# Performance work log

Hardware: AMD Instinct MI355X
Metric: run time of the kernel (lower is better)

The kernel has to match this reference:

```python
import jax, jax.numpy as jnp
import numpy as np

N = 10000
E = 640000
C = 128   # in_channels
H = 512   # hidden_dim
O = 128   # out_channels


def setup_inputs() -> dict:
    key = jax.random.key(0)
    k1, k2, k3, k4, k5, k6, k7 = jax.random.split(key, 7)
    x = jax.random.normal(k1, (N, C), dtype=jnp.float32)
    edge_index = jax.random.randint(k2, (2, E), 0, N, dtype=jnp.int64)
    # MLP params (Linear(2C, H) -> ReLU -> Linear(H, O)), torch default init scale
    w1 = jax.random.uniform(k3, (2 * C, H), jnp.float32, -1, 1) / np.sqrt(2 * C)
    b1 = jax.random.uniform(k4, (H,), jnp.float32, -1, 1) / np.sqrt(2 * C)
    w2 = jax.random.uniform(k5, (H, O), jnp.float32, -1, 1) / np.sqrt(H)
    b2 = jax.random.uniform(k6, (O,), jnp.float32, -1, 1) / np.sqrt(H)
    return {"x": x, "edge_index": edge_index, "w1": w1, "b1": b1, "w2": w2, "b2": b2}


def reference(x, edge_index, w1, b1, w2, b2):
    row, col = edge_index[0], edge_index[1]
    # scatter_mean: mean of source features x[col] into destination row
    summed = jax.ops.segment_sum(x[col], row, num_segments=N)          # [N, C]
    count = jax.ops.segment_sum(jnp.ones((E,), x.dtype), row, num_segments=N)
    neighbor_mean = summed / jnp.maximum(count, 1.0)[:, None]          # [N, C]
    h = jnp.concatenate([x, neighbor_mean], axis=1)                    # [N, 2C]
    h = jax.nn.relu(h @ w1 + b1)                                       # [N, H]
    return h @ w2 + b2                                                 # [N, O]
```

## Files before the change

kernel.cpp:

```cpp
#include <hip/hip_runtime.h>

#define C_IN 128
#define H_DIM 512
#define O_DIM 128
#define CAP   128
#define PAD   16
#define BM    32

typedef __attribute__((ext_vector_type(8))) short short8;
typedef __attribute__((ext_vector_type(4))) float f32x4;

__device__ inline unsigned short f2bf(float f) {
    unsigned int u = __float_as_uint(f);
    unsigned int r = (u + 0x7FFF + ((u >> 16) & 1)) >> 16;
    return (unsigned short)r;
}
__device__ inline float bf2f(unsigned short s) {
    return __uint_as_float(((unsigned int)s) << 16);
}

__device__ inline void tr_tile(const float* __restrict__ src, unsigned short* __restrict__ dst,
                               int R, int Ccols, int bx, int by) {
    __shared__ float tile[32][33];
    const int c0 = bx * 32, r0 = by * 32;
    const int tx = threadIdx.x & 31, ty = threadIdx.x >> 5;
#pragma unroll
    for (int i = 0; i < 32; i += 8)
        tile[ty + i][tx] = src[(long)(r0 + ty + i) * Ccols + c0 + tx];
    __syncthreads();
#pragma unroll
    for (int i = 0; i < 32; i += 8)
        dst[(long)(c0 + ty + i) * R + r0 + tx] = f2bf(tile[tx][ty + i]);
}

__global__ __launch_bounds__(256)
void prep_kernel(const float* __restrict__ w1, unsigned short* __restrict__ w1t,
                 const float* __restrict__ w2, unsigned short* __restrict__ w2t,
                 const float* __restrict__ x, unsigned short* __restrict__ h0,
                 int* __restrict__ cnt_p, int N) {
    if (blockIdx.z == 0) {
        if (blockIdx.y < (2 * C_IN) / 32) tr_tile(w1, w1t, 2 * C_IN, H_DIM, blockIdx.x, blockIdx.y);
    } else if (blockIdx.z == 1) {
        if (blockIdx.x < O_DIM / 32) tr_tile(w2, w2t, H_DIM, O_DIM, blockIdx.x, blockIdx.y);
    } else {
        const int bid = blockIdx.y * 16 + blockIdx.x;
        const int gtid = bid * 256 + threadIdx.x;
        const int nf4 = N * C_IN / 4;
        for (int i = gtid; i < nf4; i += 65536) {
            int n = i >> 5, c4 = i & 31;
            float4 v = ((const float4*)x)[i];
            ushort4 s;
            s.x = f2bf(v.x); s.y = f2bf(v.y); s.z = f2bf(v.z); s.w = f2bf(v.w);
            *(ushort4*)(h0 + (long)n * (2 * C_IN) + c4 * 4) = s;
        }
        const int n4 = N * PAD / 4;
        for (int i = gtid; i < n4; i += 65536)
            ((int4*)cnt_p)[i] = make_int4(0, 0, 0, 0);
    }
}

__global__ void fill_kernel(const int* __restrict__ ei, int* __restrict__ cnt_p,
                            unsigned short* __restrict__ bucket, int E) {
    int e = (blockIdx.x * blockDim.x + threadIdx.x) * 4;
    if (((E & 3) == 0) && e < E) {
        int4 r = *(const int4*)(ei + e);
        int4 c = *(const int4*)(ei + E + e);
        int s0 = atomicAdd(&cnt_p[r.x * PAD], 1);
        int s1 = atomicAdd(&cnt_p[r.y * PAD], 1);
        int s2 = atomicAdd(&cnt_p[r.z * PAD], 1);
        int s3 = atomicAdd(&cnt_p[r.w * PAD], 1);
        if (s0 < CAP) bucket[(long)r.x * CAP + s0] = (unsigned short)c.x;
        if (s1 < CAP) bucket[(long)r.y * CAP + s1] = (unsigned short)c.y;
        if (s2 < CAP) bucket[(long)r.z * CAP + s2] = (unsigned short)c.z;
        if (s3 < CAP) bucket[(long)r.w * CAP + s3] = (unsigned short)c.w;
    } else {
        for (int k = e; k < E && k < e + 4; k++) {
            int row = ei[k];
            int col = ei[E + k];
            int slot = atomicAdd(&cnt_p[row * PAD], 1);
            if (slot < CAP) bucket[(long)row * CAP + slot] = (unsigned short)col;
        }
    }
}

__global__ __launch_bounds__(256)
void gather_kernel(const unsigned short* __restrict__ bucket,
                   const int* __restrict__ cnt_p, unsigned short* __restrict__ h0,
                   int N) {
    const int lane = threadIdx.x & 63;
    const int n = blockIdx.x * 4 + (threadIdx.x >> 6);
    if (n >= N) return;
    const int g = lane >> 4;
    const int l16 = lane & 15;
    const int degt = cnt_p[n * PAD];
    const int deg = min(degt, CAP);

    const unsigned int bb = ((const unsigned int*)bucket)[(long)n * (CAP / 2) + lane];

    float acc[8] = {};
    int e = 0;
    for (; e + 16 <= deg; e += 16) {
        int k0 = e + g, k1 = e + 4 + g, k2 = e + 8 + g, k3 = e + 12 + g;
        int c0 = (__shfl(bb, k0 >> 1) >> ((k0 & 1) << 4)) & 0xffff;
        int c1 = (__shfl(bb, k1 >> 1) >> ((k1 & 1) << 4)) & 0xffff;
        int c2 = (__shfl(bb, k2 >> 1) >> ((k2 & 1) << 4)) & 0xffff;
        int c3 = (__shfl(bb, k3 >> 1) >> ((k3 & 1) << 4)) & 0xffff;
        short8 u0 = *(const short8*)(h0 + (long)c0 * (2 * C_IN) + l16 * 8);
        short8 u1 = *(const short8*)(h0 + (long)c1 * (2 * C_IN) + l16 * 8);
        short8 u2 = *(const short8*)(h0 + (long)c2 * (2 * C_IN) + l16 * 8);
        short8 u3 = *(const short8*)(h0 + (long)c3 * (2 * C_IN) + l16 * 8);
#pragma unroll
        for (int j = 0; j < 8; j++)
            acc[j] += (bf2f((unsigned short)u0[j]) + bf2f((unsigned short)u1[j]))
                    + (bf2f((unsigned short)u2[j]) + bf2f((unsigned short)u3[j]));
    }
    if (e + 8 <= deg) {
        int k0 = e + g, k1 = e + 4 + g;
        int c0 = (__shfl(bb, k0 >> 1) >> ((k0 & 1) << 4)) & 0xffff;
        int c1 = (__shfl(bb, k1 >> 1) >> ((k1 & 1) << 4)) & 0xffff;
        short8 u0 = *(const short8*)(h0 + (long)c0 * (2 * C_IN) + l16 * 8);
        short8 u1 = *(const short8*)(h0 + (long)c1 * (2 * C_IN) + l16 * 8);
#pragma unroll
        for (int j = 0; j < 8; j++)
            acc[j] += bf2f((unsigned short)u0[j]) + bf2f((unsigned short)u1[j]);
        e += 8;
    }
    if (e + 4 <= deg) {
        int k = e + g;
        int c = (__shfl(bb, k >> 1) >> ((k & 1) << 4)) & 0xffff;
        short8 u = *(const short8*)(h0 + (long)c * (2 * C_IN) + l16 * 8);
#pragma unroll
        for (int j = 0; j < 8; j++) acc[j] += bf2f((unsigned short)u[j]);
        e += 4;
    }
    {
        int rem = deg - e;
        int k = e + g;
        unsigned int bv = __shfl(bb, k >> 1);
        if (g < rem) {
            int c = (bv >> ((k & 1) << 4)) & 0xffff;
            short8 u = *(const short8*)(h0 + (long)c * (2 * C_IN) + l16 * 8);
#pragma unroll
            for (int j = 0; j < 8; j++) acc[j] += bf2f((unsigned short)u[j]);
        }
    }
#pragma unroll
    for (int j = 0; j < 8; j++) {
        acc[j] += __shfl_xor(acc[j], 16, 64);
        acc[j] += __shfl_xor(acc[j], 32, 64);
    }
    if (lane < 16) {
        float inv = 1.0f / fmaxf((float)degt, 1.0f);
        short8 mv;
#pragma unroll
        for (int j = 0; j < 8; j++) mv[j] = (short)f2bf(acc[j] * inv);
        *(short8*)(h0 + (long)n * (2 * C_IN) + C_IN + l16 * 8) = mv;
    }
}

__global__ __launch_bounds__(256, 3)
void fused_mlp(const unsigned short* __restrict__ h0,
               const unsigned short* __restrict__ w1t,
               const float* __restrict__ bias1,
               const unsigned short* __restrict__ w2t,
               const float* __restrict__ bias2,
               float* __restrict__ out, int M) {
    __shared__ __align__(16) unsigned short h1s[BM][520];

    const int t = threadIdx.x;
    const int m0 = blockIdx.x * BM;
    const int lane = t & 63;
    const int w = t >> 6;
    const int l16 = lane & 15;
    const int q = lane >> 4;
    const int q8 = q * 8;

    short8 a_reg[2][8];
#pragma unroll
    for (int mf = 0; mf < 2; mf++) {
        int gm = m0 + mf * 16 + l16;
        if (gm < M) {
            const unsigned short* ap = h0 + (long)gm * (2 * C_IN) + q8;
#pragma unroll
            for (int s = 0; s < 8; s++) a_reg[mf][s] = *(const short8*)(ap + s * 32);
        } else {
#pragma unroll
            for (int s = 0; s < 8; s++) a_reg[mf][s] = short8{};
        }
    }

#pragma unroll
    for (int nc = 0; nc < 4; nc++) {
        const int colbase = w * 128 + nc * 32;
        f32x4 acc[2][2] = {};
#pragma unroll
        for (int s = 0; s < 8; s++) {
            short8 b0 = *(const short8*)(w1t + (long)(colbase + l16) * 256 + s * 32 + q8);
            short8 b1 = *(const short8*)(w1t + (long)(colbase + 16 + l16) * 256 + s * 32 + q8);
            acc[0][0] = __builtin_amdgcn_mfma_f32_16x16x32_bf16(a_reg[0][s], b0, acc[0][0], 0, 0, 0);
            acc[0][1] = __builtin_amdgcn_mfma_f32_16x16x32_bf16(a_reg[0][s], b1, acc[0][1], 0, 0, 0);
            acc[1][0] = __builtin_amdgcn_mfma_f32_16x16x32_bf16(a_reg[1][s], b0, acc[1][0], 0, 0, 0);
            acc[1][1] = __builtin_amdgcn_mfma_f32_16x16x32_bf16(a_reg[1][s], b1, acc[1][1], 0, 0, 0);
        }
        float bb0 = bias1[colbase + l16];
        float bb1 = bias1[colbase + 16 + l16];
#pragma unroll
        for (int mf = 0; mf < 2; mf++) {
#pragma unroll
            for (int r = 0; r < 4; r++) {
                int m = mf * 16 + q * 4 + r;
                h1s[m][colbase + l16]      = f2bf(fmaxf(acc[mf][0][r] + bb0, 0.f));
                h1s[m][colbase + 16 + l16] = f2bf(fmaxf(acc[mf][1][r] + bb1, 0.f));
            }
        }
    }
    __syncthreads();

    f32x4 acc2[2][2] = {};
    const int wn = w * 32;
#pragma unroll
    for (int ks = 0; ks < 16; ks++) {
        short8 a0 = *(const short8*)&h1s[l16][ks * 32 + q8];
        short8 a1 = *(const short8*)&h1s[16 + l16][ks * 32 + q8];
        short8 b0 = *(const short8*)(w2t + (long)(wn + l16) * H_DIM + ks * 32 + q8);
        short8 b1 = *(const short8*)(w2t + (long)(wn + 16 + l16) * H_DIM + ks * 32 + q8);
        acc2[0][0] = __builtin_amdgcn_mfma_f32_16x16x32_bf16(a0, b0, acc2[0][0], 0, 0, 0);
        acc2[0][1] = __builtin_amdgcn_mfma_f32_16x16x32_bf16(a0, b1, acc2[0][1], 0, 0, 0);
        acc2[1][0] = __builtin_amdgcn_mfma_f32_16x16x32_bf16(a1, b0, acc2[1][0], 0, 0, 0);
        acc2[1][1] = __builtin_amdgcn_mfma_f32_16x16x32_bf16(a1, b1, acc2[1][1], 0, 0, 0);
    }
#pragma unroll
    for (int mf = 0; mf < 2; mf++) {
#pragma unroll
        for (int nf = 0; nf < 2; nf++) {
            int gn = wn + nf * 16 + l16;
            float bb = bias2[gn];
#pragma unroll
            for (int r = 0; r < 4; r++) {
                int gm = m0 + mf * 16 + q * 4 + r;
                if (gm < M) out[(long)gm * O_DIM + gn] = acc2[mf][nf][r] + bb;
            }
        }
    }
}

extern "C" void kernel_launch(void* const* d_in, const int* in_sizes, int n_in,
                              void* d_out, int out_size, void* d_ws, size_t ws_size,
                              hipStream_t stream) {
    const float* x  = (const float*)d_in[0];
    const int*   ei = (const int*)d_in[1];
    const float* w1 = (const float*)d_in[2];
    const float* b1 = (const float*)d_in[3];
    const float* w2 = (const float*)d_in[4];
    const float* b2 = (const float*)d_in[5];
    float* out = (float*)d_out;

    const int N = in_sizes[0] / C_IN;
    const int E = in_sizes[1] / 2;

    unsigned short* h0b = (unsigned short*)d_ws;
    unsigned short* w1t = h0b + (size_t)N * (2 * C_IN);
    unsigned short* w2t = w1t + (size_t)H_DIM * (2 * C_IN);
    int* cnt_p = (int*)(w2t + (size_t)O_DIM * H_DIM);
    unsigned short* bucket = (unsigned short*)(cnt_p + (size_t)N * PAD);

    prep_kernel<<<dim3(16, 16, 3), 256, 0, stream>>>(w1, w1t, w2, w2t, x, h0b, cnt_p, N);
    fill_kernel<<<(E / 4 + 255) / 256, 256, 0, stream>>>(ei, cnt_p, bucket, E);
    gather_kernel<<<(N + 3) / 4, 256, 0, stream>>>(bucket, cnt_p, h0b, N);
    fused_mlp<<<(N + BM - 1) / BM, 256, 0, stream>>>(h0b, w1t, b1, w2t, b2, out, N);
}
```

Baseline: 140.9 us.

## Fuse all stages into one persistent kernel with software grid barriers

The four launches (prep, fill, gather, MLP) become a single persistent kernel of 768 blocks. The stages are separated by atomic-counter grid barriers, and the counter zeroing moves to a hipMemsetAsync. This removes the launch gaps and tail idle between kernels. In exchange it depends on all 768 blocks being resident at once (3 per CU on 256 CUs). The barrier also has a guard timeout that could silently break ordering, and every stage now runs on a fixed grid size.

```diff
diff --git a/kernel.cpp b/kernel.cpp
--- a/kernel.cpp
+++ b/kernel.cpp
@@ -6,6 +6,7 @@
 #define CAP   128
 #define PAD   16
 #define BM    32
+#define NBLK  768
 
 typedef __attribute__((ext_vector_type(8))) short short8;
 typedef __attribute__((ext_vector_type(4))) float f32x4;
@@ -19,9 +20,24 @@
     return __uint_as_float(((unsigned int)s) << 16);
 }
 
-__device__ inline void tr_tile(const float* __restrict__ src, unsigned short* __restrict__ dst,
+__device__ inline void gbar(int* bar, int nblk) {
+    __syncthreads();
+    __builtin_amdgcn_fence(__ATOMIC_RELEASE, "agent");
+    if (threadIdx.x == 0) {
+        __hip_atomic_fetch_add(bar, 1, __ATOMIC_RELAXED, __HIP_MEMORY_SCOPE_AGENT);
+        int guard = 0;
+        while (__hip_atomic_load(bar, __ATOMIC_RELAXED, __HIP_MEMORY_SCOPE_AGENT) < nblk) {
+            __builtin_amdgcn_s_sleep(8);
+            if (++guard > (1 << 22)) break;
+        }
+    }
+    __syncthreads();
+    __builtin_amdgcn_fence(__ATOMIC_ACQUIRE, "agent");
+}
+
+__device__ inline void tr_tile(float (*tile)[33], const float* __restrict__ src,
+                               unsigned short* __restrict__ dst,
                                int R, int Ccols, int bx, int by) {
-    __shared__ float tile[32][33];
     const int c0 = bx * 32, r0 = by * 32;
     const int tx = threadIdx.x & 31, ty = threadIdx.x >> 5;
 #pragma unroll
@@ -31,216 +47,220 @@
 #pragma unroll
     for (int i = 0; i < 32; i += 8)
         dst[(long)(c0 + ty + i) * R + r0 + tx] = f2bf(tile[tx][ty + i]);
-}
-
-__global__ __launch_bounds__(256)
-void prep_kernel(const float* __restrict__ w1, unsigned short* __restrict__ w1t,
-                 const float* __restrict__ w2, unsigned short* __restrict__ w2t,
-                 const float* __restrict__ x, unsigned short* __restrict__ h0,
-                 int* __restrict__ cnt_p, int N) {
-    if (blockIdx.z == 0) {
-        if (blockIdx.y < (2 * C_IN) / 32) tr_tile(w1, w1t, 2 * C_IN, H_DIM, blockIdx.x, blockIdx.y);
-    } else if (blockIdx.z == 1) {
-        if (blockIdx.x < O_DIM / 32) tr_tile(w2, w2t, H_DIM, O_DIM, blockIdx.x, blockIdx.y);
-    } else {
-        const int bid = blockIdx.y * 16 + blockIdx.x;
-        const int gtid = bid * 256 + threadIdx.x;
-        const int nf4 = N * C_IN / 4;
-        for (int i = gtid; i < nf4; i += 65536) {
-            int n = i >> 5, c4 = i & 31;
-            float4 v = ((const float4*)x)[i];
-            ushort4 s;
-            s.x = f2bf(v.x); s.y = f2bf(v.y); s.z = f2bf(v.z); s.w = f2bf(v.w);
-            *(ushort4*)(h0 + (long)n * (2 * C_IN) + c4 * 4) = s;
-        }
-        const int n4 = N * PAD / 4;
-        for (int i = gtid; i < n4; i += 65536)
-            ((int4*)cnt_p)[i] = make_int4(0, 0, 0, 0);
-    }
-}
-
-__global__ void fill_kernel(const int* __restrict__ ei, int* __restrict__ cnt_p,
-                            unsigned short* __restrict__ bucket, int E) {
-    int e = (blockIdx.x * blockDim.x + threadIdx.x) * 4;
-    if (((E & 3) == 0) && e < E) {
-        int4 r = *(const int4*)(ei + e);
-        int4 c = *(const int4*)(ei + E + e);
-        int s0 = atomicAdd(&cnt_p[r.x * PAD], 1);
-        int s1 = atomicAdd(&cnt_p[r.y * PAD], 1);
-        int s2 = atomicAdd(&cnt_p[r.z * PAD], 1);
-        int s3 = atomicAdd(&cnt_p[r.w * PAD], 1);
-        if (s0 < CAP) bucket[(long)r.x * CAP + s0] = (unsigned short)c.x;
-        if (s1 < CAP) bucket[(long)r.y * CAP + s1] = (unsigned short)c.y;
-        if (s2 < CAP) bucket[(long)r.z * CAP + s2] = (unsigned short)c.z;
-        if (s3 < CAP) bucket[(long)r.w * CAP + s3] = (unsigned short)c.w;
-    } else {
-        for (int k = e; k < E && k < e + 4; k++) {
-            int row = ei[k];
-            int col = ei[E + k];
-            int slot = atomicAdd(&cnt_p[row * PAD], 1);
-            if (slot < CAP) bucket[(long)row * CAP + slot] = (unsigned short)col;
-        }
-    }
-}
-
-__global__ __launch_bounds__(256)
-void gather_kernel(const unsigned short* __restrict__ bucket,
-                   const int* __restrict__ cnt_p, unsigned short* __restrict__ h0,
-                   int N) {
-    const int lane = threadIdx.x & 63;
-    const int n = blockIdx.x * 4 + (threadIdx.x >> 6);
-    if (n >= N) return;
-    const int g = lane >> 4;
-    const int l16 = lane & 15;
-    const int degt = cnt_p[n * PAD];
-    const int deg = min(degt, CAP);
-
-    const unsigned int bb = ((const unsigned int*)bucket)[(long)n * (CAP / 2) + lane];
-
-    float acc[8] = {};
-    int e = 0;
-    for (; e + 16 <= deg; e += 16) {
-        int k0 = e + g, k1 = e + 4 + g, k2 = e + 8 + g, k3 = e + 12 + g;
-        int c0 = (__shfl(bb, k0 >> 1) >> ((k0 & 1) << 4)) & 0xffff;
-        int c1 = (__shfl(bb, k1 >> 1) >> ((k1 & 1) << 4)) & 0xffff;
-        int c2 = (__shfl(bb, k2 >> 1) >> ((k2 & 1) << 4)) & 0xffff;
-        int c3 = (__shfl(bb, k3 >> 1) >> ((k3 & 1) << 4)) & 0xffff;
-        short8 u0 = *(const short8*)(h0 + (long)c0 * (2 * C_IN) + l16 * 8);
-        short8 u1 = *(const short8*)(h0 + (long)c1 * (2 * C_IN) + l16 * 8);
-        short8 u2 = *(const short8*)(h0 + (long)c2 * (2 * C_IN) + l16 * 8);
-        short8 u3 = *(const short8*)(h0 + (long)c3 * (2 * C_IN) + l16 * 8);
-#pragma unroll
-        for (int j = 0; j < 8; j++)
-            acc[j] += (bf2f((unsigned short)u0[j]) + bf2f((unsigned short)u1[j]))
-                    + (bf2f((unsigned short)u2[j]) + bf2f((unsigned short)u3[j]));
-    }
-    if (e + 8 <= deg) {
-        int k0 = e + g, k1 = e + 4 + g;
-        int c0 = (__shfl(bb, k0 >> 1) >> ((k0 & 1) << 4)) & 0xffff;
-        int c1 = (__shfl(bb, k1 >> 1) >> ((k1 & 1) << 4)) & 0xffff;
-        short8 u0 = *(const short8*)(h0 + (long)c0 * (2 * C_IN) + l16 * 8);
-        short8 u1 = *(const short8*)(h0 + (long)c1 * (2 * C_IN) + l16 * 8);
-#pragma unroll
-        for (int j = 0; j < 8; j++)
-            acc[j] += bf2f((unsigned short)u0[j]) + bf2f((unsigned short)u1[j]);
-        e += 8;
-    }
-    if (e + 4 <= deg) {
-        int k = e + g;
-        int c = (__shfl(bb, k >> 1) >> ((k & 1) << 4)) & 0xffff;
-        short8 u = *(const short8*)(h0 + (long)c * (2 * C_IN) + l16 * 8);
-#pragma unroll
-        for (int j = 0; j < 8; j++) acc[j] += bf2f((unsigned short)u[j]);
-        e += 4;
-    }
-    {
-        int rem = deg - e;
-        int k = e + g;
-        unsigned int bv = __shfl(bb, k >> 1);
-        if (g < rem) {
-            int c = (bv >> ((k & 1) << 4)) & 0xffff;
-            short8 u = *(const short8*)(h0 + (long)c * (2 * C_IN) + l16 * 8);
-#pragma unroll
-            for (int j = 0; j < 8; j++) acc[j] += bf2f((unsigned short)u[j]);
-        }
-    }
-#pragma unroll
-    for (int j = 0; j < 8; j++) {
-        acc[j] += __shfl_xor(acc[j], 16, 64);
-        acc[j] += __shfl_xor(acc[j], 32, 64);
-    }
-    if (lane < 16) {
-        float inv = 1.0f / fmaxf((float)degt, 1.0f);
-        short8 mv;
-#pragma unroll
-        for (int j = 0; j < 8; j++) mv[j] = (short)f2bf(acc[j] * inv);
-        *(short8*)(h0 + (long)n * (2 * C_IN) + C_IN + l16 * 8) = mv;
-    }
+    __syncthreads();
 }
 
 __global__ __launch_bounds__(256, 3)
-void fused_mlp(const unsigned short* __restrict__ h0,
-               const unsigned short* __restrict__ w1t,
-               const float* __restrict__ bias1,
-               const unsigned short* __restrict__ w2t,
-               const float* __restrict__ bias2,
-               float* __restrict__ out, int M) {
+void fused_all(const float* __restrict__ x, const int* __restrict__ ei,
+               const float* __restrict__ w1, const float* __restrict__ bias1,
+               const float* __restrict__ w2, const float* __restrict__ bias2,
+               unsigned short* __restrict__ h0, unsigned short* __restrict__ w1t,
+               unsigned short* __restrict__ w2t, int* __restrict__ cnt_p,
+               unsigned short* __restrict__ bucket, int* __restrict__ bar,
+               float* __restrict__ out, int N, int E) {
+    __shared__ float tile[32][33];
     __shared__ __align__(16) unsigned short h1s[BM][520];
 
+    const int bid = blockIdx.x;
+    const int nblk = gridDim.x;
     const int t = threadIdx.x;
-    const int m0 = blockIdx.x * BM;
     const int lane = t & 63;
-    const int w = t >> 6;
+    const int wv = t >> 6;
     const int l16 = lane & 15;
     const int q = lane >> 4;
     const int q8 = q * 8;
 
-    short8 a_reg[2][8];
-#pragma unroll
-    for (int mf = 0; mf < 2; mf++) {
-        int gm = m0 + mf * 16 + l16;
-        if (gm < M) {
-            const unsigned short* ap = h0 + (long)gm * (2 * C_IN) + q8;
-#pragma unroll
-            for (int s = 0; s < 8; s++) a_reg[mf][s] = *(const short8*)(ap + s * 32);
+    for (int job = bid; job < 192; job += nblk) {
+        if (job < 128) {
+            tr_tile(tile, w1, w1t, 2 * C_IN, H_DIM, job & 15, job >> 4);
         } else {
-#pragma unroll
-            for (int s = 0; s < 8; s++) a_reg[mf][s] = short8{};
-        }
-    }
-
-#pragma unroll
-    for (int nc = 0; nc < 4; nc++) {
-        const int colbase = w * 128 + nc * 32;
-        f32x4 acc[2][2] = {};
-#pragma unroll
-        for (int s = 0; s < 8; s++) {
-            short8 b0 = *(const short8*)(w1t + (long)(colbase + l16) * 256 + s * 32 + q8);
-            short8 b1 = *(const short8*)(w1t + (long)(colbase + 16 + l16) * 256 + s * 32 + q8);
-            acc[0][0] = __builtin_amdgcn_mfma_f32_16x16x32_bf16(a_reg[0][s], b0, acc[0][0], 0, 0, 0);
-            acc[0][1] = __builtin_amdgcn_mfma_f32_16x16x32_bf16(a_reg[0][s], b1, acc[0][1], 0, 0, 0);
-            acc[1][0] = __builtin_amdgcn_mfma_f32_16x16x32_bf16(a_reg[1][s], b0, acc[1][0], 0, 0, 0);
-            acc[1][1] = __builtin_amdgcn_mfma_f32_16x16x32_bf16(a_reg[1][s], b1, acc[1][1], 0, 0, 0);
-        }
-        float bb0 = bias1[colbase + l16];
-        float bb1 = bias1[colbase + 16 + l16];
+            int j = job - 128;
+            tr_tile(tile, w2, w2t, H_DIM, O_DIM, j & 3, j >> 2);
+        }
+    }
+
+    {
+        const int XJ = N * C_IN / 4;
+        const int FJ = (E + 3) / 4;
+        const int gtid = bid * 256 + t;
+        const int nthr = nblk * 256;
+        const bool al = ((E & 3) == 0);
+        for (int j = gtid; j < XJ + FJ; j += nthr) {
+            if (j < XJ) {
+                int n = j >> 5, c4 = j & 31;
+                float4 v = ((const float4*)x)[j];
+                ushort4 s;
+                s.x = f2bf(v.x); s.y = f2bf(v.y); s.z = f2bf(v.z); s.w = f2bf(v.w);
+                *(ushort4*)(h0 + (long)n * (2 * C_IN) + c4 * 4) = s;
+            } else {
+                int e = (j - XJ) * 4;
+                if (al) {
+                    int4 r = *(const int4*)(ei + e);
+                    int4 c = *(const int4*)(ei + E + e);
+                    int s0 = atomicAdd(&cnt_p[r.x * PAD], 1);
+                    int s1 = atomicAdd(&cnt_p[r.y * PAD], 1);
+                    int s2 = atomicAdd(&cnt_p[r.z * PAD], 1);
+                    int s3 = atomicAdd(&cnt_p[r.w * PAD], 1);
+                    if (s0 < CAP) bucket[(long)r.x * CAP + s0] = (unsigned short)c.x;
+                    if (s1 < CAP) bucket[(long)r.y * CAP + s1] = (unsigned short)c.y;
+                    if (s2 < CAP) bucket[(long)r.z * CAP + s2] = (unsigned short)c.z;
+                    if (s3 < CAP) bucket[(long)r.w * CAP + s3] = (unsigned short)c.w;
+                } else {
+                    for (int k = e; k < E && k < e + 4; k++) {
+                        int row = ei[k];
+                        int col = ei[E + k];
+                        int slot = atomicAdd(&cnt_p[row * PAD], 1);
+                        if (slot < CAP) bucket[(long)row * CAP + slot] = (unsigned short)col;
+                    }
+                }
+            }
+        }
+    }
+
+    gbar(&bar[0], nblk);
+
+    for (int n = bid * 4 + wv; n < N; n += nblk * 4) {
+        const int g = q;
+        const int degt = cnt_p[n * PAD];
+        const int deg = min(degt, CAP);
+
+        const unsigned int bb = ((const unsigned int*)bucket)[(long)n * (CAP / 2) + lane];
+
+        float acc[8] = {};
+        int e = 0;
+        for (; e + 16 <= deg; e += 16) {
+            int k0 = e + g, k1 = e + 4 + g, k2 = e + 8 + g, k3 = e + 12 + g;
+            int c0 = (__shfl(bb, k0 >> 1) >> ((k0 & 1) << 4)) & 0xffff;
+            int c1 = (__shfl(bb, k1 >> 1) >> ((k1 & 1) << 4)) & 0xffff;
+            int c2 = (__shfl(bb, k2 >> 1) >> ((k2 & 1) << 4)) & 0xffff;
+            int c3 = (__shfl(bb, k3 >> 1) >> ((k3 & 1) << 4)) & 0xffff;
+            short8 u0 = *(const short8*)(h0 + (long)c0 * (2 * C_IN) + l16 * 8);
+            short8 u1 = *(const short8*)(h0 + (long)c1 * (2 * C_IN) + l16 * 8);
+            short8 u2 = *(const short8*)(h0 + (long)c2 * (2 * C_IN) + l16 * 8);
+            short8 u3 = *(const short8*)(h0 + (long)c3 * (2 * C_IN) + l16 * 8);
+#pragma unroll
+            for (int j = 0; j < 8; j++)
+                acc[j] += (bf2f((unsigned short)u0[j]) + bf2f((unsigned short)u1[j]))
+                        + (bf2f((unsigned short)u2[j]) + bf2f((unsigned short)u3[j]));
+        }
+        if (e + 8 <= deg) {
+            int k0 = e + g, k1 = e + 4 + g;
+            int c0 = (__shfl(bb, k0 >> 1) >> ((k0 & 1) << 4)) & 0xffff;
+            int c1 = (__shfl(bb, k1 >> 1) >> ((k1 & 1) << 4)) & 0xffff;
+            short8 u0 = *(const short8*)(h0 + (long)c0 * (2 * C_IN) + l16 * 8);
+            short8 u1 = *(const short8*)(h0 + (long)c1 * (2 * C_IN) + l16 * 8);
+#pragma unroll
+            for (int j = 0; j < 8; j++)
+                acc[j] += bf2f((unsigned short)u0[j]) + bf2f((unsigned short)u1[j]);
+            e += 8;
+        }
+        if (e + 4 <= deg) {
+            int k = e + g;
+            int c = (__shfl(bb, k >> 1) >> ((k & 1) << 4)) & 0xffff;
+            short8 u = *(const short8*)(h0 + (long)c * (2 * C_IN) + l16 * 8);
+#pragma unroll
+            for (int j = 0; j < 8; j++) acc[j] += bf2f((unsigned short)u[j]);
+            e += 4;
+        }
+        {
+            int rem = deg - e;
+            int k = e + g;
+            unsigned int bv = __shfl(bb, k >> 1);
+            if (g < rem) {
+                int c = (bv >> ((k & 1) << 4)) & 0xffff;
+                short8 u = *(const short8*)(h0 + (long)c * (2 * C_IN) + l16 * 8);
+#pragma unroll
+                for (int j = 0; j < 8; j++) acc[j] += bf2f((unsigned short)u[j]);
+            }
+        }
+#pragma unroll
+        for (int j = 0; j < 8; j++) {
+            acc[j] += __shfl_xor(acc[j], 16, 64);
+            acc[j] += __shfl_xor(acc[j], 32, 64);
+        }
+        if (lane < 16) {
+            float inv = 1.0f / fmaxf((float)degt, 1.0f);
+            short8 mv;
+#pragma unroll
+            for (int j = 0; j < 8; j++) mv[j] = (short)f2bf(acc[j] * inv);
+            *(short8*)(h0 + (long)n * (2 * C_IN) + C_IN + l16 * 8) = mv;
+        }
+    }
+
+    gbar(&bar[16], nblk);
+
+    const int MJOBS = (N + BM - 1) / BM;
+    for (int job = bid; job < MJOBS; job += nblk) {
+        const int m0 = job * BM;
+
+        short8 a_reg[2][8];
 #pragma unroll
         for (int mf = 0; mf < 2; mf++) {
-#pragma unroll
-            for (int r = 0; r < 4; r++) {
-                int m = mf * 16 + q * 4 + r;
-                h1s[m][colbase + l16]      = f2bf(fmaxf(acc[mf][0][r] + bb0, 0.f));
-                h1s[m][colbase + 16 + l16] = f2bf(fmaxf(acc[mf][1][r] + bb1, 0.f));
-            }
-        }
-    }
-    __syncthreads();
-
-    f32x4 acc2[2][2] = {};
-    const int wn = w * 32;
-#pragma unroll
-    for (int ks = 0; ks < 16; ks++) {
-        short8 a0 = *(const short8*)&h1s[l16][ks * 32 + q8];
-        short8 a1 = *(const short8*)&h1s[16 + l16][ks * 32 + q8];
-        short8 b0 = *(const short8*)(w2t + (long)(wn + l16) * H_DIM + ks * 32 + q8);
-        short8 b1 = *(const short8*)(w2t + (long)(wn + 16 + l16) * H_DIM + ks * 32 + q8);
-        acc2[0][0] = __builtin_amdgcn_mfma_f32_16x16x32_bf16(a0, b0, acc2[0][0], 0, 0, 0);
-        acc2[0][1] = __builtin_amdgcn_mfma_f32_16x16x32_bf16(a0, b1, acc2[0][1], 0, 0, 0);
-        acc2[1][0] = __builtin_amdgcn_mfma_f32_16x16x32_bf16(a1, b0, acc2[1][0], 0, 0, 0);
-        acc2[1][1] = __builtin_amdgcn_mfma_f32_16x16x32_bf16(a1, b1, acc2[1][1], 0, 0, 0);
-    }
-#pragma unroll
-    for (int mf = 0; mf < 2; mf++) {
-#pragma unroll
-        for (int nf = 0; nf < 2; nf++) {
-            int gn = wn + nf * 16 + l16;
-            float bb = bias2[gn];
-#pragma unroll
-            for (int r = 0; r < 4; r++) {
-                int gm = m0 + mf * 16 + q * 4 + r;
-                if (gm < M) out[(long)gm * O_DIM + gn] = acc2[mf][nf][r] + bb;
-            }
-        }
+            int gm = m0 + mf * 16 + l16;
+            if (gm < N) {
+                const unsigned short* ap = h0 + (long)gm * (2 * C_IN) + q8;
+#pragma unroll
+                for (int s = 0; s < 8; s++) a_reg[mf][s] = *(const short8*)(ap + s * 32);
+            } else {
+#pragma unroll
+                for (int s = 0; s < 8; s++) a_reg[mf][s] = short8{};
+            }
+        }
+
+#pragma unroll
+        for (int nc = 0; nc < 4; nc++) {
+            const int colbase = wv * 128 + nc * 32;
+            f32x4 acc[2][2] = {};
+#pragma unroll
+            for (int s = 0; s < 8; s++) {
+                short8 b0 = *(const short8*)(w1t + (long)(colbase + l16) * 256 + s * 32 + q8);
+                short8 b1 = *(const short8*)(w1t + (long)(colbase + 16 + l16) * 256 + s * 32 + q8);
+                acc[0][0] = __builtin_amdgcn_mfma_f32_16x16x32_bf16(a_reg[0][s], b0, acc[0][0], 0, 0, 0);
+                acc[0][1] = __builtin_amdgcn_mfma_f32_16x16x32_bf16(a_reg[0][s], b1, acc[0][1], 0, 0, 0);
+                acc[1][0] = __builtin_amdgcn_mfma_f32_16x16x32_bf16(a_reg[1][s], b0, acc[1][0], 0, 0, 0);
+                acc[1][1] = __builtin_amdgcn_mfma_f32_16x16x32_bf16(a_reg[1][s], b1, acc[1][1], 0, 0, 0);
+            }
+            float bb0 = bias1[colbase + l16];
+            float bb1 = bias1[colbase + 16 + l16];
+#pragma unroll
+            for (int mf = 0; mf < 2; mf++) {
+#pragma unroll
+                for (int r = 0; r < 4; r++) {
+                    int m = mf * 16 + q * 4 + r;
+                    h1s[m][colbase + l16]      = f2bf(fmaxf(acc[mf][0][r] + bb0, 0.f));
+                    h1s[m][colbase + 16 + l16] = f2bf(fmaxf(acc[mf][1][r] + bb1, 0.f));
+                }
+            }
+        }
+        __syncthreads();
+
+        f32x4 acc2[2][2] = {};
+        const int wn = wv * 32;
+#pragma unroll
+        for (int ks = 0; ks < 16; ks++) {
+            short8 a0 = *(const short8*)&h1s[l16][ks * 32 + q8];
+            short8 a1 = *(const short8*)&h1s[16 + l16][ks * 32 + q8];
+            short8 b0 = *(const short8*)(w2t + (long)(wn + l16) * H_DIM + ks * 32 + q8);
+            short8 b1 = *(const short8*)(w2t + (long)(wn + 16 + l16) * H_DIM + ks * 32 + q8);
+            acc2[0][0] = __builtin_amdgcn_mfma_f32_16x16x32_bf16(a0, b0, acc2[0][0], 0, 0, 0);
+            acc2[0][1] = __builtin_amdgcn_mfma_f32_16x16x32_bf16(a0, b1, acc2[0][1], 0, 0, 0);
+            acc2[1][0] = __builtin_amdgcn_mfma_f32_16x16x32_bf16(a1, b0, acc2[1][0], 0, 0, 0);
+            acc2[1][1] = __builtin_amdgcn_mfma_f32_16x16x32_bf16(a1, b1, acc2[1][1], 0, 0, 0);
+        }
+#pragma unroll
+        for (int mf = 0; mf < 2; mf++) {
+#pragma unroll
+            for (int nf = 0; nf < 2; nf++) {
+                int gn = wn + nf * 16 + l16;
+                float bb = bias2[gn];
+#pragma unroll
+                for (int r = 0; r < 4; r++) {
+                    int gm = m0 + mf * 16 + q * 4 + r;
+                    if (gm < N) out[(long)gm * O_DIM + gn] = acc2[mf][nf][r] + bb;
+                }
+            }
+        }
+        __syncthreads();
     }
 }
 
@@ -262,10 +282,10 @@
     unsigned short* w1t = h0b + (size_t)N * (2 * C_IN);
     unsigned short* w2t = w1t + (size_t)H_DIM * (2 * C_IN);
     int* cnt_p = (int*)(w2t + (size_t)O_DIM * H_DIM);
-    unsigned short* bucket = (unsigned short*)(cnt_p + (size_t)N * PAD);
-
-    prep_kernel<<<dim3(16, 16, 3), 256, 0, stream>>>(w1, w1t, w2, w2t, x, h0b, cnt_p, N);
-    fill_kernel<<<(E / 4 + 255) / 256, 256, 0, stream>>>(ei, cnt_p, bucket, E);
-    gather_kernel<<<(N + 3) / 4, 256, 0, stream>>>(bucket, cnt_p, h0b, N);
-    fused_mlp<<<(N + BM - 1) / BM, 256, 0, stream>>>(h0b, w1t, b1, w2t, b2, out, N);
-}
+    int* bar   = cnt_p + (size_t)N * PAD;
+    unsigned short* bucket = (unsigned short*)(bar + 64);
+
+    hipMemsetAsync(cnt_p, 0, ((size_t)N * PAD + 64) * sizeof(int), stream);
+    fused_all<<<NBLK, 256, 0, stream>>>(x, ei, w1, b1, w2, b2,
+                                        h0b, w1t, w2t, cnt_p, bucket, bar, out, N, E);
+}
```

Result: slower. 391.4 us (+177.9%).

## Fuse prep and edge-fill kernels, unroll gather by 32, drop MLP occupancy hint

Applied to the files above, without the earlier changes.

Merges the weight transpose, x-to-bf16 conversion and edge bucketing into one grid-stride kernel, and moves the counter zeroing to a hipMemsetAsync. This cuts a kernel launch and the dependency gap between prep and fill. The gather loop now issues eight neighbour loads per iteration to raise memory-level parallelism, at the cost of more registers. The fused MLP loses its min-blocks launch bound, which may change register allocation and occupancy.

```diff
diff --git a/kernel.cpp b/kernel.cpp
--- a/kernel.cpp
+++ b/kernel.cpp
@@ -34,51 +34,50 @@
 }
 
 __global__ __launch_bounds__(256)
-void prep_kernel(const float* __restrict__ w1, unsigned short* __restrict__ w1t,
-                 const float* __restrict__ w2, unsigned short* __restrict__ w2t,
-                 const float* __restrict__ x, unsigned short* __restrict__ h0,
-                 int* __restrict__ cnt_p, int N) {
-    if (blockIdx.z == 0) {
-        if (blockIdx.y < (2 * C_IN) / 32) tr_tile(w1, w1t, 2 * C_IN, H_DIM, blockIdx.x, blockIdx.y);
-    } else if (blockIdx.z == 1) {
-        if (blockIdx.x < O_DIM / 32) tr_tile(w2, w2t, H_DIM, O_DIM, blockIdx.x, blockIdx.y);
-    } else {
-        const int bid = blockIdx.y * 16 + blockIdx.x;
-        const int gtid = bid * 256 + threadIdx.x;
-        const int nf4 = N * C_IN / 4;
-        for (int i = gtid; i < nf4; i += 65536) {
-            int n = i >> 5, c4 = i & 31;
-            float4 v = ((const float4*)x)[i];
+void prep_fill(const float* __restrict__ w1, unsigned short* __restrict__ w1t,
+               const float* __restrict__ w2, unsigned short* __restrict__ w2t,
+               const float* __restrict__ x, unsigned short* __restrict__ h0,
+               const int* __restrict__ ei, int* __restrict__ cnt_p,
+               unsigned short* __restrict__ bucket, int N, int E) {
+    const int bid = blockIdx.x;
+    if (bid < 192) {
+        if (bid < 128) tr_tile(w1, w1t, 2 * C_IN, H_DIM, bid & 15, bid >> 4);
+        else { int j = bid - 128; tr_tile(w2, w2t, H_DIM, O_DIM, j & 3, j >> 2); }
+    }
+
+    const int XJ = N * C_IN / 4;
+    const int FJ = (E + 3) / 4;
+    const int gtid = bid * 256 + threadIdx.x;
+    const int nthr = gridDim.x * 256;
+    const bool al = ((E & 3) == 0);
+    for (int j = gtid; j < XJ + FJ; j += nthr) {
+        if (j < XJ) {
+            int n = j >> 5, c4 = j & 31;
+            float4 v = ((const float4*)x)[j];
             ushort4 s;
             s.x = f2bf(v.x); s.y = f2bf(v.y); s.z = f2bf(v.z); s.w = f2bf(v.w);
             *(ushort4*)(h0 + (long)n * (2 * C_IN) + c4 * 4) = s;
-        }
-        const int n4 = N * PAD / 4;
-        for (int i = gtid; i < n4; i += 65536)
-            ((int4*)cnt_p)[i] = make_int4(0, 0, 0, 0);
-    }
-}
-
-__global__ void fill_kernel(const int* __restrict__ ei, int* __restrict__ cnt_p,
-                            unsigned short* __restrict__ bucket, int E) {
-    int e = (blockIdx.x * blockDim.x + threadIdx.x) * 4;
-    if (((E & 3) == 0) && e < E) {
-        int4 r = *(const int4*)(ei + e);
-        int4 c = *(const int4*)(ei + E + e);
-        int s0 = atomicAdd(&cnt_p[r.x * PAD], 1);
-        int s1 = atomicAdd(&cnt_p[r.y * PAD], 1);
-        int s2 = atomicAdd(&cnt_p[r.z * PAD], 1);
-        int s3 = atomicAdd(&cnt_p[r.w * PAD], 1);
-        if (s0 < CAP) bucket[(long)r.x * CAP + s0] = (unsigned short)c.x;
-        if (s1 < CAP) bucket[(long)r.y * CAP + s1] = (unsigned short)c.y;
-        if (s2 < CAP) bucket[(long)r.z * CAP + s2] = (unsigned short)c.z;
-        if (s3 < CAP) bucket[(long)r.w * CAP + s3] = (unsigned short)c.w;
-    } else {
-        for (int k = e; k < E && k < e + 4; k++) {
-            int row = ei[k];
-            int col = ei[E + k];
-            int slot = atomicAdd(&cnt_p[row * PAD], 1);
-            if (slot < CAP) bucket[(long)row * CAP + slot] = (unsigned short)col;
+        } else {
+            int e = (j - XJ) * 4;
+            if (al) {
+                int4 r = *(const int4*)(ei + e);
+                int4 c = *(const int4*)(ei + E + e);
+                int s0 = atomicAdd(&cnt_p[r.x * PAD], 1);
+                int s1 = atomicAdd(&cnt_p[r.y * PAD], 1);
+                int s2 = atomicAdd(&cnt_p[r.z * PAD], 1);
+                int s3 = atomicAdd(&cnt_p[r.w * PAD], 1);
+                if (s0 < CAP) bucket[(long)r.x * CAP + s0] = (unsigned short)c.x;
+                if (s1 < CAP) bucket[(long)r.y * CAP + s1] = (unsigned short)c.y;
+                if (s2 < CAP) bucket[(long)r.z * CAP + s2] = (unsigned short)c.z;
+                if (s3 < CAP) bucket[(long)r.w * CAP + s3] = (unsigned short)c.w;
+            } else {
+                for (int k = e; k < E && k < e + 4; k++) {
+                    int row = ei[k];
+                    int col = ei[E + k];
+                    int slot = atomicAdd(&cnt_p[row * PAD], 1);
+                    if (slot < CAP) bucket[(long)row * CAP + slot] = (unsigned short)col;
+                }
+            }
         }
     }
 }
@@ -99,7 +98,27 @@
 
     float acc[8] = {};
     int e = 0;
-    for (; e + 16 <= deg; e += 16) {
+    for (; e + 32 <= deg; e += 32) {
+        int c[8];
+#pragma unroll
+        for (int i = 0; i < 8; i++) {
+            int k = e + 4 * i + g;
+            c[i] = (__shfl(bb, k >> 1) >> ((k & 1) << 4)) & 0xffff;
+        }
+        short8 u[8];
+#pragma unroll
+        for (int i = 0; i < 8; i++)
+            u[i] = *(const short8*)(h0 + (long)c[i] * (2 * C_IN) + l16 * 8);
+#pragma unroll
+        for (int j = 0; j < 8; j++) {
+            float s0 = bf2f((unsigned short)u[0][j]) + bf2f((unsigned short)u[1][j]);
+            float s1 = bf2f((unsigned short)u[2][j]) + bf2f((unsigned short)u[3][j]);
+            float s2 = bf2f((unsigned short)u[4][j]) + bf2f((unsigned short)u[5][j]);
+            float s3 = bf2f((unsigned short)u[6][j]) + bf2f((unsigned short)u[7][j]);
+            acc[j] += (s0 + s1) + (s2 + s3);
+        }
+    }
+    if (e + 16 <= deg) {
         int k0 = e + g, k1 = e + 4 + g, k2 = e + 8 + g, k3 = e + 12 + g;
         int c0 = (__shfl(bb, k0 >> 1) >> ((k0 & 1) << 4)) & 0xffff;
         int c1 = (__shfl(bb, k1 >> 1) >> ((k1 & 1) << 4)) & 0xffff;
@@ -113,6 +132,7 @@
         for (int j = 0; j < 8; j++)
             acc[j] += (bf2f((unsigned short)u0[j]) + bf2f((unsigned short)u1[j]))
                     + (bf2f((unsigned short)u2[j]) + bf2f((unsigned short)u3[j]));
+        e += 16;
     }
     if (e + 8 <= deg) {
         int k0 = e + g, k1 = e + 4 + g;
@@ -158,7 +178,7 @@
     }
 }
 
-__global__ __launch_bounds__(256, 3)
+__global__ __launch_bounds__(256)
 void fused_mlp(const unsigned short* __restrict__ h0,
                const unsigned short* __restrict__ w1t,
                const float* __restrict__ bias1,
@@ -264,8 +284,8 @@
     int* cnt_p = (int*)(w2t + (size_t)O_DIM * H_DIM);
     unsigned short* bucket = (unsigned short*)(cnt_p + (size_t)N * PAD);
 
-    prep_kernel<<<dim3(16, 16, 3), 256, 0, stream>>>(w1, w1t, w2, w2t, x, h0b, cnt_p, N);
-    fill_kernel<<<(E / 4 + 255) / 256, 256, 0, stream>>>(ei, cnt_p, bucket, E);
+    hipMemsetAsync(cnt_p, 0, (size_t)N * PAD * sizeof(int), stream);
+    prep_fill<<<1024, 256, 0, stream>>>(w1, w1t, w2, w2t, x, h0b, ei, cnt_p, bucket, N, E);
     gather_kernel<<<(N + 3) / 4, 256, 0, stream>>>(bucket, cnt_p, h0b, N);
     fused_mlp<<<(N + BM - 1) / BM, 256, 0, stream>>>(h0b, w1t, b1, w2t, b2, out, N);
 }
```

New measurement: 139.1 us. About the same (-1.2%).
